# Optimization experiments

Measured on AMD Instinct MI355X. Metric: run time of the kernel, lower is better.

## Reference

```python
import jax, jax.numpy as jnp
import numpy as np

N_NODES = 10000
N_EDGES = 640000
IN_CH, HID, OUT_CH = 128, 128, 64


def _gcn_conv(x, edge_index, edge_weight, W, b, n_nodes):
    # PyG GCNConv (default add_self_loops=True, normalize=True, bias=True):
    #   A_hat = A + I ; D = rowsum(A_hat) ; norm_e = D^-1/2[src] * w_e * D^-1/2[dst]
    #   out[dst] += norm_e * (x @ W)[src] ; out += b
    src, dst = edge_index[0], edge_index[1]
    loop = jnp.arange(n_nodes, dtype=edge_index.dtype)
    src = jnp.concatenate([src, loop])
    dst = jnp.concatenate([dst, loop])
    w = jnp.concatenate([edge_weight, jnp.ones((n_nodes,), edge_weight.dtype)])
    deg = jax.ops.segment_sum(w, dst, num_segments=n_nodes)  # scatter on col
    dinv = jnp.where(deg > 0, jax.lax.rsqrt(deg), 0.0).astype(x.dtype)
    norm = dinv[src] * w * dinv[dst]  # [E+N]
    xw = x @ W  # dense GEMM [N, out]
    msg = norm[:, None] * xw[src]  # gather + scale [E+N, out]
    out = jax.ops.segment_sum(msg, dst, num_segments=n_nodes)  # scatter-add
    return out + b


def setup_inputs() -> dict:
    key = jax.random.key(0)
    ks = jax.random.split(key, 8)
    x = jax.random.normal(ks[0], (N_NODES, IN_CH), dtype=jnp.float32)
    edge_index = jax.random.randint(ks[1], (2, N_EDGES), 0, N_NODES, dtype=jnp.int64)
    edge_weight = jax.random.uniform(ks[2], (N_EDGES,), dtype=jnp.float32)
    W1 = jax.random.normal(ks[3], (IN_CH, HID), dtype=jnp.float32) * 0.05
    b1 = jnp.zeros((HID,), jnp.float32)
    W2 = jax.random.normal(ks[4], (HID, OUT_CH), dtype=jnp.float32) * 0.05
    b2 = jnp.zeros((OUT_CH,), jnp.float32)
    return {"x": x, "edge_index": edge_index, "edge_weight": edge_weight,
            "W1": W1, "b1": b1, "W2": W2, "b2": b2}


def reference(x, edge_index, edge_weight, W1, b1, W2, b2):
    h = _gcn_conv(x, edge_index, edge_weight, W1, b1, N_NODES)
    h = jax.nn.relu(h)
    out = _gcn_conv(h, edge_index, edge_weight, W2, b2, N_NODES)
    return out
```

## Files before the change

### kernel.cpp

```cpp
#include <hip/hip_runtime.h>
#include <math.h>

#define N_NODES 10000
#define N_EDGES 640000
#define ELLW    192

#define CHUNKS  128
#define CHUNK_E 5000
#define GB      625

typedef unsigned long long ull;
typedef unsigned int uint;
typedef unsigned short ushort;
typedef unsigned char uchar;

#define FIXED_SCALE 262144.0f


__device__ __forceinline__ float bf_lo(uint u) { return __uint_as_float(u << 16); }
__device__ __forceinline__ float bf_hi(uint u) { return __uint_as_float(u & 0xffff0000u); }
__device__ __forceinline__ ushort f2bf(float v) {
    uint u = __float_as_uint(v);
    uint r = u + 0x7fffu + ((u >> 16) & 1u);
    return (ushort)(r >> 16);
}

__global__ __launch_bounds__(256) void kernelA(const int* __restrict__ ei,
                                               const float* __restrict__ ew,
                                               uint* __restrict__ sd32,
                                               uint* __restrict__ blockcnt,
                                               const float* __restrict__ x,
                                               const float* __restrict__ W1,
                                               ushort* __restrict__ xw1b) {
    __shared__ uint smem[N_NODES];
    const int tid = threadIdx.x;
    if (blockIdx.x < CHUNKS) {
        const int c = blockIdx.x;
        __shared__ int sflag;
        if (tid == 0) sflag = 0;
        for (int i = tid; i < N_NODES; i += 256) smem[i] = 0u;
        __syncthreads();
        int a = (tid < 64) ? ei[2 * (c * CHUNK_E + tid) + 1] : 0;
        if (a) atomicOr(&sflag, 1);
        __syncthreads();
        const int f = sflag;
        const ull* ei64 = (const ull*)ei;
        for (int k = tid; k < CHUNK_E; k += 256) {
            int e = c * CHUNK_E + k;
            int s, d;
            if (f) { s = ei[e];        d = ei[N_EDGES + e]; }
            else   { s = (int)ei64[e]; d = (int)ei64[N_EDGES + e]; }
            float w = ew[e];
            uint fx = (uint)(w * FIXED_SCALE + 0.5f);
            uint old = atomicAdd(&smem[d], (1u << 24) | fx);
            uint r = (old >> 24) & 15u;
            sd32[e] = (r << 28) | ((uint)d << 14) | (uint)s;
        }
        __syncthreads();
        for (int i = tid; i < N_NODES; i += 256)
            blockcnt[c * N_NODES + i] = smem[i];
    } else {
        constexpr int K = 128, TM = 16, KT = 32, NCOL = 128, RPT = 8;
        float* sA = (float*)smem;
        float* sB = sA + TM * (KT + 1);
        int blk = blockIdx.x - CHUNKS;
        int c = tid % NCOL, rr = tid / NCOL;
        int row0 = blk * TM;
        float acc[RPT];
#pragma unroll
        for (int r = 0; r < RPT; ++r) acc[r] = 0.0f;
        for (int k0 = 0; k0 < K; k0 += KT) {
            for (int i = tid; i < TM * KT; i += 256) {
                int r = i / KT, k = i % KT;
                int gr = row0 + r;
                sA[r * (KT + 1) + k] = (gr < N_NODES) ? x[gr * K + k0 + k] : 0.0f;
            }
            for (int i = tid; i < KT * NCOL; i += 256) {
                int k = i / NCOL, cc = i % NCOL;
                sB[k * NCOL + cc] = W1[(k0 + k) * NCOL + cc];
            }
            __syncthreads();
#pragma unroll
            for (int k = 0; k < KT; ++k) {
                float b = sB[k * NCOL + c];
#pragma unroll
                for (int r = 0; r < RPT; ++r)
                    acc[r] += sA[(rr * RPT + r) * (KT + 1) + k] * b;
            }
            __syncthreads();
        }
#pragma unroll
        for (int r = 0; r < RPT; ++r) {
            int gr = row0 + rr * RPT + r;
            if (gr < N_NODES) xw1b[gr * NCOL + c] = f2bf(acc[r]);
        }
    }
}

__global__ __launch_bounds__(256) void scanB(const uint* __restrict__ blockcnt,
                                             uchar* __restrict__ base8,
                                             int* __restrict__ cnt_arr,
                                             float* __restrict__ dinv,
                                             const float* __restrict__ W2,
                                             uint* __restrict__ w2pg) {
    if (blockIdx.x >= 40) {
        int i = (blockIdx.x - 40) * 256 + threadIdx.x;
        int k2 = i >> 6, cc = i & 63;
        uint lo = (uint)f2bf(W2[(2 * k2) * 64 + cc]);
        uint hi = (uint)f2bf(W2[(2 * k2 + 1) * 64 + cc]);
        w2pg[i] = lo | (hi << 16);
        return;
    }
    int n = blockIdx.x * 256 + threadIdx.x;
    if (n >= N_NODES) return;
    uint wsum = 0;
    int run = 0;
#pragma unroll 8
    for (int c = 0; c < CHUNKS; ++c) {
        uint v = blockcnt[c * N_NODES + n];
        base8[c * N_NODES + n] = (uchar)run;
        run += (int)(v >> 24);
        wsum += v & 0xffffffu;
    }
    cnt_arr[n] = run;
    float dg = 1.0f + (float)wsum * (1.0f / FIXED_SCALE);
    dinv[n] = (float)(1.0 / sqrt((double)dg));
}

__global__ __launch_bounds__(256) void fillC(const uint* __restrict__ sd32,
                                             const float* __restrict__ ew,
                                             const uchar* __restrict__ base8,
                                             const float* __restrict__ dinv,
                                             ull* __restrict__ epack) {
    const int gid = blockIdx.x * 256 + threadIdx.x;
    const int stride = gridDim.x * 256;
    for (int e = gid; e < N_EDGES; e += stride) {
        uint sd = sd32[e];
        int s = (int)(sd & 0x3fffu);
        int d = (int)((sd >> 14) & 0x3fffu);
        int r = (int)(sd >> 28);
        int c = e / CHUNK_E;
        float nrm = dinv[s] * ew[e] * dinv[d];
        int slot = (int)base8[c * N_NODES + d] + r;
        if (slot < ELLW)
            epack[d * ELLW + slot] = ((ull)__float_as_uint(nrm) << 32) | (ull)(uint)s;
    }
}

__global__ __launch_bounds__(256, 8) void aggC(const ushort* __restrict__ xw1b,
                                               const ull* __restrict__ epack,
                                               const int* __restrict__ cnt_arr,
                                               const float* __restrict__ dinv,
                                               const float* __restrict__ b1,
                                               const uint* __restrict__ w2pg,
                                               ushort* __restrict__ xw2b) {
    __shared__ float hl[4][128];
    __shared__ uint w2p[64 * 64];
    const uint* __restrict__ xw32 = (const uint*)xw1b;
    const int tid = threadIdx.x;
    int l = tid & 63;
    int wv = tid >> 6;
    int node = blockIdx.x * 4 + wv;

    for (int i = tid; i < 64 * 64; i += 256) w2p[i] = w2pg[i];

    int cnt = __builtin_amdgcn_readfirstlane(cnt_arr[node]);
    if (cnt > ELLW) cnt = ELLW;
    float dn = dinv[node];
    float d2 = dn * dn;
    uint su = xw32[node * 64 + l];
    float acc0 = d2 * bf_lo(su);
    float acc1 = d2 * bf_hi(su);
    const ull* ep = epack + (long)node * ELLW;
    int j = 0;
    for (; j + 8 <= cnt; j += 8) {
        ulonglong2 v0 = *(const ulonglong2*)(ep + j);
        ulonglong2 v1 = *(const ulonglong2*)(ep + j + 2);
        ulonglong2 v2 = *(const ulonglong2*)(ep + j + 4);
        ulonglong2 v3 = *(const ulonglong2*)(ep + j + 6);
        uint u0 = xw32[(uint)v0.x * 64 + l];
        uint u1 = xw32[(uint)v0.y * 64 + l];
        uint u2 = xw32[(uint)v1.x * 64 + l];
        uint u3 = xw32[(uint)v1.y * 64 + l];
        uint u4 = xw32[(uint)v2.x * 64 + l];
        uint u5 = xw32[(uint)v2.y * 64 + l];
        uint u6 = xw32[(uint)v3.x * 64 + l];
        uint u7 = xw32[(uint)v3.y * 64 + l];
        float n0 = __uint_as_float((uint)(v0.x >> 32));
        float n1 = __uint_as_float((uint)(v0.y >> 32));
        float n2 = __uint_as_float((uint)(v1.x >> 32));
        float n3 = __uint_as_float((uint)(v1.y >> 32));
        float n4 = __uint_as_float((uint)(v2.x >> 32));
        float n5 = __uint_as_float((uint)(v2.y >> 32));
        float n6 = __uint_as_float((uint)(v3.x >> 32));
        float n7 = __uint_as_float((uint)(v3.y >> 32));
        acc0 = fmaf(n0, bf_lo(u0), acc0); acc1 = fmaf(n0, bf_hi(u0), acc1);
        acc0 = fmaf(n1, bf_lo(u1), acc0); acc1 = fmaf(n1, bf_hi(u1), acc1);
        acc0 = fmaf(n2, bf_lo(u2), acc0); acc1 = fmaf(n2, bf_hi(u2), acc1);
        acc0 = fmaf(n3, bf_lo(u3), acc0); acc1 = fmaf(n3, bf_hi(u3), acc1);
        acc0 = fmaf(n4, bf_lo(u4), acc0); acc1 = fmaf(n4, bf_hi(u4), acc1);
        acc0 = fmaf(n5, bf_lo(u5), acc0); acc1 = fmaf(n5, bf_hi(u5), acc1);
        acc0 = fmaf(n6, bf_lo(u6), acc0); acc1 = fmaf(n6, bf_hi(u6), acc1);
        acc0 = fmaf(n7, bf_lo(u7), acc0); acc1 = fmaf(n7, bf_hi(u7), acc1);
    }
    for (; j + 2 <= cnt; j += 2) {
        ulonglong2 vv = *(const ulonglong2*)(ep + j);
        uint u0 = xw32[(uint)vv.x * 64 + l];
        uint u1 = xw32[(uint)vv.y * 64 + l];
        float n0 = __uint_as_float((uint)(vv.x >> 32));
        float n1 = __uint_as_float((uint)(vv.y >> 32));
        acc0 = fmaf(n0, bf_lo(u0), acc0); acc1 = fmaf(n0, bf_hi(u0), acc1);
        acc0 = fmaf(n1, bf_lo(u1), acc0); acc1 = fmaf(n1, bf_hi(u1), acc1);
    }
    if (j < cnt) {
        ull v = ep[j];
        uint u = xw32[(uint)v * 64 + l];
        float n = __uint_as_float((uint)(v >> 32));
        acc0 = fmaf(n, bf_lo(u), acc0);
        acc1 = fmaf(n, bf_hi(u), acc1);
    }
    float2 bb = ((const float2*)b1)[l];
    hl[wv][2 * l]     = fmaxf(acc0 + bb.x, 0.0f);
    hl[wv][2 * l + 1] = fmaxf(acc1 + bb.y, 0.0f);
    __syncthreads();

    float acc = 0.0f;
#pragma unroll 8
    for (int k2 = 0; k2 < 64; ++k2) {
        uint w = w2p[k2 * 64 + l];
        acc = fmaf(hl[wv][2 * k2],     bf_lo(w), acc);
        acc = fmaf(hl[wv][2 * k2 + 1], bf_hi(w), acc);
    }
    xw2b[node * 64 + l] = f2bf(acc);
}

__global__ __launch_bounds__(256) void agg2(const ushort* __restrict__ xw2b,
                                            const ull* __restrict__ epack,
                                            const int* __restrict__ cnt_arr,
                                            const float* __restrict__ dinv,
                                            const float* __restrict__ b2,
                                            float* __restrict__ out) {
    const uint* __restrict__ xw32 = (const uint*)xw2b;
    int lane = threadIdx.x & 63;
    int half = lane >> 5;
    int q = lane & 31;
    int pair = blockIdx.x * 4 + (threadIdx.x >> 6);
    int A = pair * 2, B = A + 1;
    int cntA = __builtin_amdgcn_readfirstlane(cnt_arr[A]);
    int cntB = __builtin_amdgcn_readfirstlane(cnt_arr[B]);
    if (cntA > ELLW) cntA = ELLW;
    if (cntB > ELLW) cntB = ELLW;
    int myn = half ? B : A;
    int mycnt = half ? cntB : cntA;
    float dn = dinv[myn];
    float d2 = dn * dn;
    uint su = xw32[myn * 32 + q];
    float acc0 = d2 * bf_lo(su);
    float acc1 = d2 * bf_hi(su);
    const ull* epA = epack + (long)A * ELLW;
    const ull* epB = epack + (long)B * ELLW;
    int mx = cntA > cntB ? cntA : cntB;
    int j = 0;
    for (; j + 8 <= mx; j += 8) {
        ulonglong2 a0 = *(const ulonglong2*)(epA + j);
        ulonglong2 a1 = *(const ulonglong2*)(epA + j + 2);
        ulonglong2 a2 = *(const ulonglong2*)(epA + j + 4);
        ulonglong2 a3 = *(const ulonglong2*)(epA + j + 6);
        ulonglong2 b0 = *(const ulonglong2*)(epB + j);
        ulonglong2 b1v = *(const ulonglong2*)(epB + j + 2);
        ulonglong2 b2v = *(const ulonglong2*)(epB + j + 4);
        ulonglong2 b3 = *(const ulonglong2*)(epB + j + 6);
        ull e0 = half ? b0.x : a0.x;
        ull e1 = half ? b0.y : a0.y;
        ull e2 = half ? b1v.x : a1.x;
        ull e3 = half ? b1v.y : a1.y;
        ull e4 = half ? b2v.x : a2.x;
        ull e5 = half ? b2v.y : a2.y;
        ull e6 = half ? b3.x : a3.x;
        ull e7 = half ? b3.y : a3.y;
        uint u0 = xw32[((uint)e0 & 0xffffu) * 32 + q];
        uint u1 = xw32[((uint)e1 & 0xffffu) * 32 + q];
        uint u2 = xw32[((uint)e2 & 0xffffu) * 32 + q];
        uint u3 = xw32[((uint)e3 & 0xffffu) * 32 + q];
        uint u4 = xw32[((uint)e4 & 0xffffu) * 32 + q];
        uint u5 = xw32[((uint)e5 & 0xffffu) * 32 + q];
        uint u6 = xw32[((uint)e6 & 0xffffu) * 32 + q];
        uint u7 = xw32[((uint)e7 & 0xffffu) * 32 + q];
        float n0 = (j     < mycnt) ? __uint_as_float((uint)(e0 >> 32)) : 0.0f;
        float n1 = (j + 1 < mycnt) ? __uint_as_float((uint)(e1 >> 32)) : 0.0f;
        float n2 = (j + 2 < mycnt) ? __uint_as_float((uint)(e2 >> 32)) : 0.0f;
        float n3 = (j + 3 < mycnt) ? __uint_as_float((uint)(e3 >> 32)) : 0.0f;
        float n4 = (j + 4 < mycnt) ? __uint_as_float((uint)(e4 >> 32)) : 0.0f;
        float n5 = (j + 5 < mycnt) ? __uint_as_float((uint)(e5 >> 32)) : 0.0f;
        float n6 = (j + 6 < mycnt) ? __uint_as_float((uint)(e6 >> 32)) : 0.0f;
        float n7 = (j + 7 < mycnt) ? __uint_as_float((uint)(e7 >> 32)) : 0.0f;
        acc0 = fmaf(n0, bf_lo(u0), acc0); acc1 = fmaf(n0, bf_hi(u0), acc1);
        acc0 = fmaf(n1, bf_lo(u1), acc0); acc1 = fmaf(n1, bf_hi(u1), acc1);
        acc0 = fmaf(n2, bf_lo(u2), acc0); acc1 = fmaf(n2, bf_hi(u2), acc1);
        acc0 = fmaf(n3, bf_lo(u3), acc0); acc1 = fmaf(n3, bf_hi(u3), acc1);
        acc0 = fmaf(n4, bf_lo(u4), acc0); acc1 = fmaf(n4, bf_hi(u4), acc1);
        acc0 = fmaf(n5, bf_lo(u5), acc0); acc1 = fmaf(n5, bf_hi(u5), acc1);
        acc0 = fmaf(n6, bf_lo(u6), acc0); acc1 = fmaf(n6, bf_hi(u6), acc1);
        acc0 = fmaf(n7, bf_lo(u7), acc0); acc1 = fmaf(n7, bf_hi(u7), acc1);
    }
    for (; j < mx; ++j) {
        ull vA = epA[j], vB = epB[j];
        ull v = half ? vB : vA;
        uint s = (uint)v & 0xffffu;
        float n = (j < mycnt) ? __uint_as_float((uint)(v >> 32)) : 0.0f;
        uint u = xw32[s * 32 + q];
        acc0 = fmaf(n, bf_lo(u), acc0);
        acc1 = fmaf(n, bf_hi(u), acc1);
    }
    float2 bb = ((const float2*)b2)[q];
    float2 o;
    o.x = acc0 + bb.x;
    o.y = acc1 + bb.y;
    ((float2*)out)[myn * 32 + q] = o;
}

extern "C" void kernel_launch(void* const* d_in, const int* in_sizes, int n_in,
                              void* d_out, int out_size, void* d_ws, size_t ws_size,
                              hipStream_t stream) {
    const float* x  = (const float*)d_in[0];
    const int*   ei = (const int*)d_in[1];
    const float* ew = (const float*)d_in[2];
    const float* W1 = (const float*)d_in[3];
    const float* b1 = (const float*)d_in[4];
    const float* W2 = (const float*)d_in[5];
    const float* b2 = (const float*)d_in[6];
    float* out = (float*)d_out;

    char* ws = (char*)d_ws;
    ushort* xw1b    = (ushort*)(ws + 0);
    ushort* xw2b    = (ushort*)(ws + 5120000);
    ull*    epack   = (ull*)   (ws + 6400000);
    uint*   blockcnt= (uint*)  (ws + 21760000);
    uchar*  base8   = (uchar*) (ws + 26880000);
    uint*   sd32    = (uint*)  (ws + 28800000);
    int*    cnt_arr = (int*)   (ws + 31360000);
    float*  dinv    = (float*) (ws + 31400000);
    uint*   w2pg    = (uint*)  (ws + 31440000);

    kernelA<<<CHUNKS + GB, 256, 0, stream>>>(ei, ew, sd32, blockcnt, x, W1, xw1b);
    scanB<<<56, 256, 0, stream>>>(blockcnt, base8, cnt_arr, dinv, W2, w2pg);
    fillC<<<512, 256, 0, stream>>>(sd32, ew, base8, dinv, epack);
    aggC<<<2500, 256, 0, stream>>>(xw1b, epack, cnt_arr, dinv, b1, w2pg, xw2b);
    agg2<<<1250, 256, 0, stream>>>(xw2b, epack, cnt_arr, dinv, b2, out);
}
```

Before: 156.4 us.

## Software-pipeline edge loads in aggregation kernels and vectorize GEMM shared reads

Both aggregation kernels now prefetch the next 8 packed edges while gathering features for the current 8, which hides the latency of the edge-list load behind the gathers. agg2 reads only its own node's edge row instead of loading two rows and selecting between them, and aggC moves its first edge load ahead of the W2 shared-memory fill. The GEMM part of kernelA uses float4 shared reads with a padded stride and unrolls k by 4, fillC launches more blocks, and aggC's launch_bounds occupancy hint drops from 8 to 4. Extra live registers from the prefetch may lower occupancy.

```diff
diff --git a/kernel.cpp b/kernel.cpp
--- a/kernel.cpp
+++ b/kernel.cpp
@@ -32,7 +32,7 @@
                                                const float* __restrict__ x,
                                                const float* __restrict__ W1,
                                                ushort* __restrict__ xw1b) {
-    __shared__ uint smem[N_NODES];
+    __shared__ __align__(16) uint smem[N_NODES];
     const int tid = threadIdx.x;
     if (blockIdx.x < CHUNKS) {
         const int c = blockIdx.x;
@@ -60,9 +60,9 @@
         for (int i = tid; i < N_NODES; i += 256)
             blockcnt[c * N_NODES + i] = smem[i];
     } else {
-        constexpr int K = 128, TM = 16, KT = 32, NCOL = 128, RPT = 8;
+        constexpr int K = 128, TM = 16, KT = 32, NCOL = 128, RPT = 8, LDA = KT + 4;
         float* sA = (float*)smem;
-        float* sB = sA + TM * (KT + 1);
+        float* sB = sA + TM * LDA;
         int blk = blockIdx.x - CHUNKS;
         int c = tid % NCOL, rr = tid / NCOL;
         int row0 = blk * TM;
@@ -73,7 +73,7 @@
             for (int i = tid; i < TM * KT; i += 256) {
                 int r = i / KT, k = i % KT;
                 int gr = row0 + r;
-                sA[r * (KT + 1) + k] = (gr < N_NODES) ? x[gr * K + k0 + k] : 0.0f;
+                sA[r * LDA + k] = (gr < N_NODES) ? x[gr * K + k0 + k] : 0.0f;
             }
             for (int i = tid; i < KT * NCOL; i += 256) {
                 int k = i / NCOL, cc = i % NCOL;
@@ -81,11 +81,19 @@
             }
             __syncthreads();
 #pragma unroll
-            for (int k = 0; k < KT; ++k) {
-                float b = sB[k * NCOL + c];
+            for (int k = 0; k < KT; k += 4) {
+                float b0 = sB[(k + 0) * NCOL + c];
+                float b1 = sB[(k + 1) * NCOL + c];
+                float b2 = sB[(k + 2) * NCOL + c];
+                float b3 = sB[(k + 3) * NCOL + c];
 #pragma unroll
-                for (int r = 0; r < RPT; ++r)
-                    acc[r] += sA[(rr * RPT + r) * (KT + 1) + k] * b;
+                for (int r = 0; r < RPT; ++r) {
+                    const float4 av = *(const float4*)&sA[(rr * RPT + r) * LDA + k];
+                    acc[r] = fmaf(av.x, b0, acc[r]);
+                    acc[r] = fmaf(av.y, b1, acc[r]);
+                    acc[r] = fmaf(av.z, b2, acc[r]);
+                    acc[r] = fmaf(av.w, b3, acc[r]);
+                }
             }
             __syncthreads();
         }
@@ -147,7 +155,7 @@
     }
 }
 
-__global__ __launch_bounds__(256, 8) void aggC(const ushort* __restrict__ xw1b,
+__global__ __launch_bounds__(256, 4) void aggC(const ushort* __restrict__ xw1b,
                                                const ull* __restrict__ epack,
                                                const int* __restrict__ cnt_arr,
                                                const float* __restrict__ dinv,
@@ -162,46 +170,87 @@
     int wv = tid >> 6;
     int node = blockIdx.x * 4 + wv;
 
-    for (int i = tid; i < 64 * 64; i += 256) w2p[i] = w2pg[i];
-
     int cnt = __builtin_amdgcn_readfirstlane(cnt_arr[node]);
     if (cnt > ELLW) cnt = ELLW;
+    const ull* ep = epack + (long)node * ELLW;
+
+    ulonglong2 c0, c1, c2, c3;
+    const bool has8 = (cnt >= 8);
+    if (has8) {
+        c0 = *(const ulonglong2*)(ep + 0);
+        c1 = *(const ulonglong2*)(ep + 2);
+        c2 = *(const ulonglong2*)(ep + 4);
+        c3 = *(const ulonglong2*)(ep + 6);
+    }
+
+    for (int i = tid; i < 64 * 64; i += 256) w2p[i] = w2pg[i];
+
     float dn = dinv[node];
     float d2 = dn * dn;
     uint su = xw32[node * 64 + l];
     float acc0 = d2 * bf_lo(su);
     float acc1 = d2 * bf_hi(su);
-    const ull* ep = epack + (long)node * ELLW;
+
     int j = 0;
-    for (; j + 8 <= cnt; j += 8) {
-        ulonglong2 v0 = *(const ulonglong2*)(ep + j);
-        ulonglong2 v1 = *(const ulonglong2*)(ep + j + 2);
-        ulonglong2 v2 = *(const ulonglong2*)(ep + j + 4);
-        ulonglong2 v3 = *(const ulonglong2*)(ep + j + 6);
-        uint u0 = xw32[(uint)v0.x * 64 + l];
-        uint u1 = xw32[(uint)v0.y * 64 + l];
-        uint u2 = xw32[(uint)v1.x * 64 + l];
-        uint u3 = xw32[(uint)v1.y * 64 + l];
-        uint u4 = xw32[(uint)v2.x * 64 + l];
-        uint u5 = xw32[(uint)v2.y * 64 + l];
-        uint u6 = xw32[(uint)v3.x * 64 + l];
-        uint u7 = xw32[(uint)v3.y * 64 + l];
-        float n0 = __uint_as_float((uint)(v0.x >> 32));
-        float n1 = __uint_as_float((uint)(v0.y >> 32));
-        float n2 = __uint_as_float((uint)(v1.x >> 32));
-        float n3 = __uint_as_float((uint)(v1.y >> 32));
-        float n4 = __uint_as_float((uint)(v2.x >> 32));
-        float n5 = __uint_as_float((uint)(v2.y >> 32));
-        float n6 = __uint_as_float((uint)(v3.x >> 32));
-        float n7 = __uint_as_float((uint)(v3.y >> 32));
-        acc0 = fmaf(n0, bf_lo(u0), acc0); acc1 = fmaf(n0, bf_hi(u0), acc1);
-        acc0 = fmaf(n1, bf_lo(u1), acc0); acc1 = fmaf(n1, bf_hi(u1), acc1);
-        acc0 = fmaf(n2, bf_lo(u2), acc0); acc1 = fmaf(n2, bf_hi(u2), acc1);
-        acc0 = fmaf(n3, bf_lo(u3), acc0); acc1 = fmaf(n3, bf_hi(u3), acc1);
-        acc0 = fmaf(n4, bf_lo(u4), acc0); acc1 = fmaf(n4, bf_hi(u4), acc1);
-        acc0 = fmaf(n5, bf_lo(u5), acc0); acc1 = fmaf(n5, bf_hi(u5), acc1);
-        acc0 = fmaf(n6, bf_lo(u6), acc0); acc1 = fmaf(n6, bf_hi(u6), acc1);
-        acc0 = fmaf(n7, bf_lo(u7), acc0); acc1 = fmaf(n7, bf_hi(u7), acc1);
+    if (has8) {
+        for (; j + 16 <= cnt; j += 8) {
+            uint u0 = xw32[(uint)c0.x * 64 + l];
+            uint u1 = xw32[(uint)c0.y * 64 + l];
+            uint u2 = xw32[(uint)c1.x * 64 + l];
+            uint u3 = xw32[(uint)c1.y * 64 + l];
+            uint u4 = xw32[(uint)c2.x * 64 + l];
+            uint u5 = xw32[(uint)c2.y * 64 + l];
+            uint u6 = xw32[(uint)c3.x * 64 + l];
+            uint u7 = xw32[(uint)c3.y * 64 + l];
+            ulonglong2 p0 = *(const ulonglong2*)(ep + j + 8);
+            ulonglong2 p1 = *(const ulonglong2*)(ep + j + 10);
+            ulonglong2 p2 = *(const ulonglong2*)(ep + j + 12);
+            ulonglong2 p3 = *(const ulonglong2*)(ep + j + 14);
+            float n0 = __uint_as_float((uint)(c0.x >> 32));
+            float n1 = __uint_as_float((uint)(c0.y >> 32));
+            float n2 = __uint_as_float((uint)(c1.x >> 32));
+            float n3 = __uint_as_float((uint)(c1.y >> 32));
+            float n4 = __uint_as_float((uint)(c2.x >> 32));
+            float n5 = __uint_as_float((uint)(c2.y >> 32));
+            float n6 = __uint_as_float((uint)(c3.x >> 32));
+            float n7 = __uint_as_float((uint)(c3.y >> 32));
+            acc0 = fmaf(n0, bf_lo(u0), acc0); acc1 = fmaf(n0, bf_hi(u0), acc1);
+            acc0 = fmaf(n1, bf_lo(u1), acc0); acc1 = fmaf(n1, bf_hi(u1), acc1);
+            acc0 = fmaf(n2, bf_lo(u2), acc0); acc1 = fmaf(n2, bf_hi(u2), acc1);
+            acc0 = fmaf(n3, bf_lo(u3), acc0); acc1 = fmaf(n3, bf_hi(u3), acc1);
+            acc0 = fmaf(n4, bf_lo(u4), acc0); acc1 = fmaf(n4, bf_hi(u4), acc1);
+            acc0 = fmaf(n5, bf_lo(u5), acc0); acc1 = fmaf(n5, bf_hi(u5), acc1);
+            acc0 = fmaf(n6, bf_lo(u6), acc0); acc1 = fmaf(n6, bf_hi(u6), acc1);
+            acc0 = fmaf(n7, bf_lo(u7), acc0); acc1 = fmaf(n7, bf_hi(u7), acc1);
+            c0 = p0; c1 = p1; c2 = p2; c3 = p3;
+        }
+        {
+            uint u0 = xw32[(uint)c0.x * 64 + l];
+            uint u1 = xw32[(uint)c0.y * 64 + l];
+            uint u2 = xw32[(uint)c1.x * 64 + l];
+            uint u3 = xw32[(uint)c1.y * 64 + l];
+            uint u4 = xw32[(uint)c2.x * 64 + l];
+            uint u5 = xw32[(uint)c2.y * 64 + l];
+            uint u6 = xw32[(uint)c3.x * 64 + l];
+            uint u7 = xw32[(uint)c3.y * 64 + l];
+            float n0 = __uint_as_float((uint)(c0.x >> 32));
+            float n1 = __uint_as_float((uint)(c0.y >> 32));
+            float n2 = __uint_as_float((uint)(c1.x >> 32));
+            float n3 = __uint_as_float((uint)(c1.y >> 32));
+            float n4 = __uint_as_float((uint)(c2.x >> 32));
+            float n5 = __uint_as_float((uint)(c2.y >> 32));
+            float n6 = __uint_as_float((uint)(c3.x >> 32));
+            float n7 = __uint_as_float((uint)(c3.y >> 32));
+            acc0 = fmaf(n0, bf_lo(u0), acc0); acc1 = fmaf(n0, bf_hi(u0), acc1);
+            acc0 = fmaf(n1, bf_lo(u1), acc0); acc1 = fmaf(n1, bf_hi(u1), acc1);
+            acc0 = fmaf(n2, bf_lo(u2), acc0); acc1 = fmaf(n2, bf_hi(u2), acc1);
+            acc0 = fmaf(n3, bf_lo(u3), acc0); acc1 = fmaf(n3, bf_hi(u3), acc1);
+            acc0 = fmaf(n4, bf_lo(u4), acc0); acc1 = fmaf(n4, bf_hi(u4), acc1);
+            acc0 = fmaf(n5, bf_lo(u5), acc0); acc1 = fmaf(n5, bf_hi(u5), acc1);
+            acc0 = fmaf(n6, bf_lo(u6), acc0); acc1 = fmaf(n6, bf_hi(u6), acc1);
+            acc0 = fmaf(n7, bf_lo(u7), acc0); acc1 = fmaf(n7, bf_hi(u7), acc1);
+            j += 8;
+        }
     }
     for (; j + 2 <= cnt; j += 2) {
         ulonglong2 vv = *(const ulonglong2*)(ep + j);
@@ -257,55 +306,75 @@
     uint su = xw32[myn * 32 + q];
     float acc0 = d2 * bf_lo(su);
     float acc1 = d2 * bf_hi(su);
-    const ull* epA = epack + (long)A * ELLW;
-    const ull* epB = epack + (long)B * ELLW;
+    const ull* ep = epack + (long)myn * ELLW;
     int mx = cntA > cntB ? cntA : cntB;
     int j = 0;
-    for (; j + 8 <= mx; j += 8) {
-        ulonglong2 a0 = *(const ulonglong2*)(epA + j);
-        ulonglong2 a1 = *(const ulonglong2*)(epA + j + 2);
-        ulonglong2 a2 = *(const ulonglong2*)(epA + j + 4);
-        ulonglong2 a3 = *(const ulonglong2*)(epA + j + 6);
-        ulonglong2 b0 = *(const ulonglong2*)(epB + j);
-        ulonglong2 b1v = *(const ulonglong2*)(epB + j + 2);
-        ulonglong2 b2v = *(const ulonglong2*)(epB + j + 4);
-        ulonglong2 b3 = *(const ulonglong2*)(epB + j + 6);
-        ull e0 = half ? b0.x : a0.x;
-        ull e1 = half ? b0.y : a0.y;
-        ull e2 = half ? b1v.x : a1.x;
-        ull e3 = half ? b1v.y : a1.y;
-        ull e4 = half ? b2v.x : a2.x;
-        ull e5 = half ? b2v.y : a2.y;
-        ull e6 = half ? b3.x : a3.x;
-        ull e7 = half ? b3.y : a3.y;
-        uint u0 = xw32[((uint)e0 & 0xffffu) * 32 + q];
-        uint u1 = xw32[((uint)e1 & 0xffffu) * 32 + q];
-        uint u2 = xw32[((uint)e2 & 0xffffu) * 32 + q];
-        uint u3 = xw32[((uint)e3 & 0xffffu) * 32 + q];
-        uint u4 = xw32[((uint)e4 & 0xffffu) * 32 + q];
-        uint u5 = xw32[((uint)e5 & 0xffffu) * 32 + q];
-        uint u6 = xw32[((uint)e6 & 0xffffu) * 32 + q];
-        uint u7 = xw32[((uint)e7 & 0xffffu) * 32 + q];
-        float n0 = (j     < mycnt) ? __uint_as_float((uint)(e0 >> 32)) : 0.0f;
-        float n1 = (j + 1 < mycnt) ? __uint_as_float((uint)(e1 >> 32)) : 0.0f;
-        float n2 = (j + 2 < mycnt) ? __uint_as_float((uint)(e2 >> 32)) : 0.0f;
-        float n3 = (j + 3 < mycnt) ? __uint_as_float((uint)(e3 >> 32)) : 0.0f;
-        float n4 = (j + 4 < mycnt) ? __uint_as_float((uint)(e4 >> 32)) : 0.0f;
-        float n5 = (j + 5 < mycnt) ? __uint_as_float((uint)(e5 >> 32)) : 0.0f;
-        float n6 = (j + 6 < mycnt) ? __uint_as_float((uint)(e6 >> 32)) : 0.0f;
-        float n7 = (j + 7 < mycnt) ? __uint_as_float((uint)(e7 >> 32)) : 0.0f;
-        acc0 = fmaf(n0, bf_lo(u0), acc0); acc1 = fmaf(n0, bf_hi(u0), acc1);
-        acc0 = fmaf(n1, bf_lo(u1), acc0); acc1 = fmaf(n1, bf_hi(u1), acc1);
-        acc0 = fmaf(n2, bf_lo(u2), acc0); acc1 = fmaf(n2, bf_hi(u2), acc1);
-        acc0 = fmaf(n3, bf_lo(u3), acc0); acc1 = fmaf(n3, bf_hi(u3), acc1);
-        acc0 = fmaf(n4, bf_lo(u4), acc0); acc1 = fmaf(n4, bf_hi(u4), acc1);
-        acc0 = fmaf(n5, bf_lo(u5), acc0); acc1 = fmaf(n5, bf_hi(u5), acc1);
-        acc0 = fmaf(n6, bf_lo(u6), acc0); acc1 = fmaf(n6, bf_hi(u6), acc1);
-        acc0 = fmaf(n7, bf_lo(u7), acc0); acc1 = fmaf(n7, bf_hi(u7), acc1);
+    if (mx >= 8) {
+        ulonglong2 c0 = *(const ulonglong2*)(ep + 0);
+        ulonglong2 c1 = *(const ulonglong2*)(ep + 2);
+        ulonglong2 c2 = *(const ulonglong2*)(ep + 4);
+        ulonglong2 c3 = *(const ulonglong2*)(ep + 6);
+        for (; j + 16 <= mx; j += 8) {
+            uint u0 = xw32[((uint)c0.x & 0xffffu) * 32 + q];
+            uint u1 = xw32[((uint)c0.y & 0xffffu) * 32 + q];
+            uint u2 = xw32[((uint)c1.x & 0xffffu) * 32 + q];
+            uint u3 = xw32[((uint)c1.y & 0xffffu) * 32 + q];
+            uint u4 = xw32[((uint)c2.x & 0xffffu) * 32 + q];
+            uint u5 = xw32[((uint)c2.y & 0xffffu) * 32 + q];
+            uint u6 = xw32[((uint)c3.x & 0xffffu) * 32 + q];
+            uint u7 = xw32[((uint)c3.y & 0xffffu) * 32 + q];
+            ulonglong2 p0 = *(const ulonglong2*)(ep + j + 8);
+            ulonglong2 p1 = *(const ulonglong2*)(ep + j + 10);
+            ulonglong2 p2 = *(const ulonglong2*)(ep + j + 12);
+            ulonglong2 p3 = *(const ulonglong2*)(ep + j + 14);
+            float n0 = (j     < mycnt) ? __uint_as_float((uint)(c0.x >> 32)) : 0.0f;
+            float n1 = (j + 1 < mycnt) ? __uint_as_float((uint)(c0.y >> 32)) : 0.0f;
+            float n2 = (j + 2 < mycnt) ? __uint_as_float((uint)(c1.x >> 32)) : 0.0f;
+            float n3 = (j + 3 < mycnt) ? __uint_as_float((uint)(c1.y >> 32)) : 0.0f;
+            float n4 = (j + 4 < mycnt) ? __uint_as_float((uint)(c2.x >> 32)) : 0.0f;
+            float n5 = (j + 5 < mycnt) ? __uint_as_float((uint)(c2.y >> 32)) : 0.0f;
+            float n6 = (j + 6 < mycnt) ? __uint_as_float((uint)(c3.x >> 32)) : 0.0f;
+            float n7 = (j + 7 < mycnt) ? __uint_as_float((uint)(c3.y >> 32)) : 0.0f;
+            acc0 = fmaf(n0, bf_lo(u0), acc0); acc1 = fmaf(n0, bf_hi(u0), acc1);
+            acc0 = fmaf(n1, bf_lo(u1), acc0); acc1 = fmaf(n1, bf_hi(u1), acc1);
+            acc0 = fmaf(n2, bf_lo(u2), acc0); acc1 = fmaf(n2, bf_hi(u2), acc1);
+            acc0 = fmaf(n3, bf_lo(u3), acc0); acc1 = fmaf(n3, bf_hi(u3), acc1);
+            acc0 = fmaf(n4, bf_lo(u4), acc0); acc1 = fmaf(n4, bf_hi(u4), acc1);
+            acc0 = fmaf(n5, bf_lo(u5), acc0); acc1 = fmaf(n5, bf_hi(u5), acc1);
+            acc0 = fmaf(n6, bf_lo(u6), acc0); acc1 = fmaf(n6, bf_hi(u6), acc1);
+            acc0 = fmaf(n7, bf_lo(u7), acc0); acc1 = fmaf(n7, bf_hi(u7), acc1);
+            c0 = p0; c1 = p1; c2 = p2; c3 = p3;
+        }
+        {
+            uint u0 = xw32[((uint)c0.x & 0xffffu) * 32 + q];
+            uint u1 = xw32[((uint)c0.y & 0xffffu) * 32 + q];
+            uint u2 = xw32[((uint)c1.x & 0xffffu) * 32 + q];
+            uint u3 = xw32[((uint)c1.y & 0xffffu) * 32 + q];
+            uint u4 = xw32[((uint)c2.x & 0xffffu) * 32 + q];
+            uint u5 = xw32[((uint)c2.y & 0xffffu) * 32 + q];
+            uint u6 = xw32[((uint)c3.x & 0xffffu) * 32 + q];
+            uint u7 = xw32[((uint)c3.y & 0xffffu) * 32 + q];
+            float n0 = (j     < mycnt) ? __uint_as_float((uint)(c0.x >> 32)) : 0.0f;
+            float n1 = (j + 1 < mycnt) ? __uint_as_float((uint)(c0.y >> 32)) : 0.0f;
+            float n2 = (j + 2 < mycnt) ? __uint_as_float((uint)(c1.x >> 32)) : 0.0f;
+            float n3 = (j + 3 < mycnt) ? __uint_as_float((uint)(c1.y >> 32)) : 0.0f;
+            float n4 = (j + 4 < mycnt) ? __uint_as_float((uint)(c2.x >> 32)) : 0.0f;
+            float n5 = (j + 5 < mycnt) ? __uint_as_float((uint)(c2.y >> 32)) : 0.0f;
+            float n6 = (j + 6 < mycnt) ? __uint_as_float((uint)(c3.x >> 32)) : 0.0f;
+            float n7 = (j + 7 < mycnt) ? __uint_as_float((uint)(c3.y >> 32)) : 0.0f;
+            acc0 = fmaf(n0, bf_lo(u0), acc0); acc1 = fmaf(n0, bf_hi(u0), acc1);
+            acc0 = fmaf(n1, bf_lo(u1), acc0); acc1 = fmaf(n1, bf_hi(u1), acc1);
+            acc0 = fmaf(n2, bf_lo(u2), acc0); acc1 = fmaf(n2, bf_hi(u2), acc1);
+            acc0 = fmaf(n3, bf_lo(u3), acc0); acc1 = fmaf(n3, bf_hi(u3), acc1);
+            acc0 = fmaf(n4, bf_lo(u4), acc0); acc1 = fmaf(n4, bf_hi(u4), acc1);
+            acc0 = fmaf(n5, bf_lo(u5), acc0); acc1 = fmaf(n5, bf_hi(u5), acc1);
+            acc0 = fmaf(n6, bf_lo(u6), acc0); acc1 = fmaf(n6, bf_hi(u6), acc1);
+            acc0 = fmaf(n7, bf_lo(u7), acc0); acc1 = fmaf(n7, bf_hi(u7), acc1);
+            j += 8;
+        }
     }
     for (; j < mx; ++j) {
-        ull vA = epA[j], vB = epB[j];
-        ull v = half ? vB : vA;
+        ull v = ep[j];
         uint s = (uint)v & 0xffffu;
         float n = (j < mycnt) ? __uint_as_float((uint)(v >> 32)) : 0.0f;
         uint u = xw32[s * 32 + q];
@@ -344,7 +413,7 @@
 
     kernelA<<<CHUNKS + GB, 256, 0, stream>>>(ei, ew, sd32, blockcnt, x, W1, xw1b);
     scanB<<<56, 256, 0, stream>>>(blockcnt, base8, cnt_arr, dinv, W2, w2pg);
-    fillC<<<512, 256, 0, stream>>>(sd32, ew, base8, dinv, epack);
+    fillC<<<2500, 256, 0, stream>>>(sd32, ew, base8, dinv, epack);
     aggC<<<2500, 256, 0, stream>>>(xw1b, epack, cnt_arr, dinv, b1, w2pg, xw2b);
     agg2<<<1250, 256, 0, stream>>>(xw2b, epack, cnt_arr, dinv, b2, out);
 }
```

New measurement: 146.7 us. 6.2% less time.
